# Performance work log

Measured on AMD Instinct MI355X. Metric: run time of the kernel, lower is better.

Reference implementation:

```python
import jax, jax.numpy as jnp
import numpy as np

B, D, H, E, TOP_K = 4096, 1024, 4096, 8, 2
EPS = 2.220446049250313e-16  # float64 machine eps, as in the torch source


def setup_inputs() -> dict:
    key = jax.random.key(0)
    k0, k1, k2, k3 = jax.random.split(key, 4)
    x = jax.random.normal(k0, (B, 1, D), dtype=jnp.float32)
    # torch inits w_gate to zeros (degenerate ties in topk); use small random for a meaningful test
    w_gate = jax.random.normal(k1, (D, E), dtype=jnp.float32) * 0.02
    W1 = jax.random.normal(k2, (E, D, H), dtype=jnp.float32) * (1.0 / np.sqrt(D))
    b1 = jnp.zeros((E, H), dtype=jnp.float32)
    W2 = jax.random.normal(k3, (E, H, D), dtype=jnp.float32) * (1.0 / np.sqrt(H))
    b2 = jnp.zeros((E, D), dtype=jnp.float32)
    loss_coef = jnp.float32(0.01)
    return {"x": x, "w_gate": w_gate, "W1": W1, "b1": b1, "W2": W2, "b2": b2,
            "loss_coef": loss_coef}


def _cv_squared(v, eps=1e-10):
    # torch .var() is unbiased (ddof=1)
    return jnp.var(v, ddof=1) / (jnp.mean(v) ** 2 + eps)


def reference(x, w_gate, W1, b1, W2, b2, loss_coef):
    n_tok = x.shape[0]
    flat = x.reshape(n_tok, -1)                      # [B, D]

    # --- top-k gating ---
    logits = flat @ w_gate                           # [B, E]
    top_logits, top_idx = jax.lax.top_k(logits, TOP_K)
    top_gates = jax.nn.softmax(top_logits, axis=1)   # softmax over the top-k logits only
    gates = jnp.zeros_like(logits).at[jnp.arange(n_tok)[:, None], top_idx].set(top_gates)

    # --- load-balancing loss ---
    importance = gates.sum(axis=0)                               # [E]
    load = (gates > 0).sum(axis=0).astype(jnp.float32)           # [E]
    balancing_loss = (_cv_squared(importance) + _cv_squared(load)) * loss_coef

    # --- per-expert FFN (dense equivalent of sort/dispatch: zero gates kill non-routed terms) ---
    h = jax.nn.relu(jnp.einsum('bd,edh->beh', flat, W1) + b1)    # [B, E, H]
    o = jnp.einsum('beh,ehd->bed', h, W2) + b2                   # [B, E, D]

    # --- combine: sum_e gate * exp(expert_out), then log (exp/log trick) ---
    combined = jnp.einsum('bed,be->bd', jnp.exp(o), gates)       # [B, D]
    combined = jnp.where(combined == 0, EPS, combined)
    y = jnp.log(combined)
    return y, balancing_loss
```

## Files before the change

### kernel.cpp

```cpp
#include <hip/hip_runtime.h>


typedef __attribute__((ext_vector_type(8))) short short8;
typedef __attribute__((ext_vector_type(4))) float f32x4;

#define B_TOK 4096
#define D_DIM 1024
#define H_DIM 4096
#define N_EXP 8
#define H_HALF 2048

__device__ __forceinline__ unsigned short f2bf(float f) {
  unsigned int u = __float_as_uint(f);
  u += 0x7fffu + ((u >> 16) & 1u);
  return (unsigned short)(u >> 16);
}
__device__ __forceinline__ float bf2f(unsigned short s) {
  return __uint_as_float(((unsigned int)s) << 16);
}

__device__ __forceinline__ void async_ld16(const void* g, void* l) {
  __builtin_amdgcn_global_load_lds(
      (const __attribute__((address_space(1))) void*)g,
      (__attribute__((address_space(3))) void*)l, 16, 0, 0);
}

__global__ __launch_bounds__(256) void convert_x_kernel(const float* __restrict__ x,
                                                        unsigned short* __restrict__ xb) {
  const size_t i = ((size_t)blockIdx.x * 256 + threadIdx.x) * 4;
  float4 v = *(const float4*)(x + i);
  ushort4 r;
  r.x = f2bf(v.x); r.y = f2bf(v.y); r.z = f2bf(v.z); r.w = f2bf(v.w);
  *(ushort4*)(xb + i) = r;
}

__global__ __launch_bounds__(256) void gating_kernel(
    const float* __restrict__ x, const float* __restrict__ wg,
    int* __restrict__ tok_e, float* __restrict__ tok_g) {
  const int lane = threadIdx.x & 63;
  const int t = blockIdx.x * 4 + (threadIdx.x >> 6);
  const float* xr = x + (size_t)t * D_DIM;
  double acc[8] = {0, 0, 0, 0, 0, 0, 0, 0};
  for (int d = lane; d < D_DIM; d += 64) {
    double xv = (double)xr[d];
    const float4 w0 = *(const float4*)(wg + d * 8);
    const float4 w1 = *(const float4*)(wg + d * 8 + 4);
    acc[0] += xv * (double)w0.x; acc[1] += xv * (double)w0.y;
    acc[2] += xv * (double)w0.z; acc[3] += xv * (double)w0.w;
    acc[4] += xv * (double)w1.x; acc[5] += xv * (double)w1.y;
    acc[6] += xv * (double)w1.z; acc[7] += xv * (double)w1.w;
  }
#pragma unroll
  for (int e = 0; e < 8; ++e) {
    double v = acc[e];
#pragma unroll
    for (int m = 32; m > 0; m >>= 1) v += __shfl_xor(v, m, 64);
    acc[e] = v;
  }
  if (lane == 0) {
    double b1v = -1e300, b2v = -1e300;
    int i1 = 0, i2 = 0;
#pragma unroll
    for (int e = 0; e < 8; ++e) {
      double v = acc[e];
      if (v > b1v) { b2v = b1v; i2 = i1; b1v = v; i1 = e; }
      else if (v > b2v) { b2v = v; i2 = e; }
    }
    float ex = expf((float)b2v - (float)b1v);
    float den = 1.f + ex;
    tok_e[2 * t] = i1; tok_e[2 * t + 1] = i2;
    tok_g[2 * t] = 1.f / den; tok_g[2 * t + 1] = ex / den;
  }
}

__global__ __launch_bounds__(1024) void route_kernel(
    const int* __restrict__ tok_e, const float* __restrict__ tok_g,
    int* __restrict__ tok_p, int* __restrict__ bucket,
    int* __restrict__ counts, int* __restrict__ offs,
    const float* __restrict__ coef, float* __restrict__ loss_out) {
  __shared__ int wavecnt[16][8];
  __shared__ int wavebase[16][8];
  __shared__ int run[8];
  __shared__ float impl[8];
  const int tid = threadIdx.x, lane = tid & 63, wv = tid >> 6;
  if (tid < 8) { run[tid] = 0; impl[tid] = 0.f; }
  __syncthreads();
  for (int c = 0; c < 8; ++c) {
    const int i = c * 1024 + tid;
    const int e = tok_e[i];
    const float g = tok_g[i];
    int rank = 0;
#pragma unroll
    for (int ee = 0; ee < 8; ++ee) {
      unsigned long long m = __ballot(e == ee);
      if (e == ee) rank = __popcll(m & ((1ull << lane) - 1ull));
      float s = (e == ee) ? g : 0.f;
#pragma unroll
      for (int o = 32; o > 0; o >>= 1) s += __shfl_xor(s, o, 64);
      if (lane == 0) {
        wavecnt[wv][ee] = __popcll(m);
        impl[ee] += 0.f;
        atomicAdd(&impl[ee], s);
      }
    }
    __syncthreads();
    if (tid < 8) {
      int base = run[tid];
      for (int w = 0; w < 16; ++w) { wavebase[w][tid] = base; base += wavecnt[w][tid]; }
      run[tid] = base;
    }
    __syncthreads();
    const int pos = wavebase[wv][e] + rank;
    tok_p[i] = pos;
    bucket[e * B_TOK + pos] = i >> 1;
  }
  __syncthreads();
  if (tid == 0) {
    int o = 0;
    double mi = 0, ml = 0;
    for (int e = 0; e < 8; ++e) {
      counts[e] = run[e]; offs[e] = o; o += run[e];
      mi += (double)impl[e]; ml += (double)run[e];
    }
    offs[8] = o;
    mi *= 0.125; ml *= 0.125;
    double vi = 0, vl = 0;
    for (int e = 0; e < 8; ++e) {
      double di = (double)impl[e] - mi; vi += di * di;
      double dl = (double)run[e]  - ml; vl += dl * dl;
    }
    vi /= 7.0; vl /= 7.0;
    *loss_out = (float)((vi / (mi * mi + 1e-10) + vl / (ml * ml + 1e-10)) * (double)coef[0]);
  }
}

__global__ __launch_bounds__(256) void transpose_w_kernel(
    const float* __restrict__ W, unsigned short* __restrict__ Wt,
    int ND_src, int k_base, int n_base, int KD_out,
    size_t w_stride_e, size_t wt_stride_e) {
  const int e = blockIdx.z;
  const int kt = blockIdx.x * 64;
  const int nt = blockIdx.y * 64;
  const float* We = W + (size_t)e * w_stride_e + (size_t)(k_base + kt) * ND_src + n_base + nt;
  unsigned short* Wte = Wt + (size_t)e * wt_stride_e + (size_t)nt * KD_out + kt;
  __shared__ unsigned int Ul[64][36];
  const int t = threadIdx.x;
  const int cb = (t & 15) * 4;
#pragma unroll
  for (int j = 0; j < 2; ++j) {
    const int p = (t >> 4) + j * 16;
    float4 f0 = *(const float4*)(We + (size_t)(2 * p) * ND_src + cb);
    float4 f1 = *(const float4*)(We + (size_t)(2 * p + 1) * ND_src + cb);
#pragma unroll
    for (int i2 = 0; i2 < 4; ++i2) {
      unsigned int u = (unsigned int)f2bf(((const float*)&f0)[i2]) |
                       ((unsigned int)f2bf(((const float*)&f1)[i2]) << 16);
      Ul[cb + i2][p] = u;
    }
  }
  __syncthreads();
  const int on = t >> 2;
  const int om = (t & 3) * 8;
  uint4 a = *(const uint4*)&Ul[on][om];
  uint4 b = *(const uint4*)&Ul[on][om + 4];
  uint4* dst = (uint4*)(Wte + (size_t)on * KD_out + om * 2);
  dst[0] = a; dst[1] = b;
}

template <int KDIM, int NDIM, bool GATHER, bool RELU, bool ACCUM>
__global__ __launch_bounds__(256) void grouped_gemm(
    const unsigned short* __restrict__ A, const unsigned short* __restrict__ Bt,
    const float* __restrict__ bias, int biasN,
    const int* __restrict__ counts, const int* __restrict__ offs,
    const int* __restrict__ bucket, unsigned short* __restrict__ Out, int outN) {
  const int e = blockIdx.z;
  const int n_e = counts[e];
  const int row0 = blockIdx.y * 128;
  if (row0 >= n_e) return;
  const int m_cnt = min(128, n_e - row0);
  const int n0 = blockIdx.x * 128;
  const int slot0 = offs[e] + row0;

  __shared__ unsigned short Alds[128][32];
  __shared__ unsigned short Blds[128][32];
  __shared__ int toklds[128];

  const int tid = threadIdx.x;
  const int lane = tid & 63;
  const int wid = tid >> 6;
  const int q = lane >> 4, l15 = lane & 15;
  const int wm = (wid >> 1) * 64, wn = (wid & 1) * 64;

  if (GATHER) {
    if (tid < 128) toklds[tid] = bucket[e * B_TOK + row0 + min(tid, m_cnt - 1)];
    __syncthreads();
  }
  const int r0 = tid >> 2;
  const int kc = (tid & 3) * 8;
  size_t ga0, ga1;
  if (GATHER) {
    ga0 = (size_t)toklds[r0] * KDIM + kc;
    ga1 = (size_t)toklds[r0 + 64] * KDIM + kc;
  } else {
    ga0 = (size_t)(slot0 + min(r0, m_cnt - 1)) * KDIM + kc;
    ga1 = (size_t)(slot0 + min(r0 + 64, m_cnt - 1)) * KDIM + kc;
  }
  const unsigned short* bbase =
      Bt + (size_t)e * NDIM * KDIM + (size_t)(n0 + r0) * KDIM + kc;
  char* aldsw = (char*)Alds + wid * 1024;
  char* bldsw = (char*)Blds + wid * 1024;

  f32x4 acc[4][4] = {};
  for (int k0 = 0; k0 < KDIM; k0 += 32) {
    async_ld16(A + ga0 + k0, aldsw);
    async_ld16(A + ga1 + k0, aldsw + 4096);
    async_ld16(bbase + k0, bldsw);
    async_ld16(bbase + (size_t)64 * KDIM + k0, bldsw + 4096);
    __syncthreads();
    short8 af[4], bfr[4];
#pragma unroll
    for (int mi = 0; mi < 4; ++mi) af[mi] = *(const short8*)&Alds[wm + mi * 16 + l15][q * 8];
#pragma unroll
    for (int ni = 0; ni < 4; ++ni) bfr[ni] = *(const short8*)&Blds[wn + ni * 16 + l15][q * 8];
#pragma unroll
    for (int mi = 0; mi < 4; ++mi)
#pragma unroll
      for (int ni = 0; ni < 4; ++ni)
        acc[mi][ni] = __builtin_amdgcn_mfma_f32_16x16x32_bf16(af[mi], bfr[ni], acc[mi][ni], 0, 0, 0);
    __syncthreads();
  }

  const float* be = bias + (size_t)e * biasN + n0;
#pragma unroll
  for (int ni = 0; ni < 4; ++ni) {
    const int c = wn + ni * 16 + l15;
    const float bv = ACCUM ? 0.f : be[c];
#pragma unroll
    for (int mi = 0; mi < 4; ++mi) {
      const int rb = wm + mi * 16 + q * 4;
#pragma unroll
      for (int rg = 0; rg < 4; ++rg) {
        const int r = rb + rg;
        if (r < m_cnt) {
          float v = acc[mi][ni][rg] + bv;
          if (RELU) v = fmaxf(v, 0.f);
          unsigned short* op = Out + (size_t)(slot0 + r) * outN + n0 + c;
          if (ACCUM) v += bf2f(*op);
          *op = f2bf(v);
        }
      }
    }
  }
}

__device__ __forceinline__ float comb1(float a, float b, float g1, float g2) {
  float c = g1 * expf(a) + g2 * expf(b);
  if (c == 0.f) c = 2.220446049250313e-16f;
  return logf(c);
}

__global__ __launch_bounds__(256) void combine_kernel(
    const unsigned short* __restrict__ o_buf, const int* __restrict__ offs,
    const int* __restrict__ tok_e, const int* __restrict__ tok_p,
    const float* __restrict__ tok_g, float* __restrict__ y) {
  const int t = blockIdx.x;
  const int e1 = tok_e[2 * t], e2 = tok_e[2 * t + 1];
  const int s1 = offs[e1] + tok_p[2 * t];
  const int s2 = offs[e2] + tok_p[2 * t + 1];
  const float g1 = tok_g[2 * t], g2 = tok_g[2 * t + 1];
  const int i = threadIdx.x * 4;
  ushort4 a4 = *(const ushort4*)(o_buf + (size_t)s1 * D_DIM + i);
  ushort4 b4 = *(const ushort4*)(o_buf + (size_t)s2 * D_DIM + i);
  float4 r;
  r.x = comb1(bf2f(a4.x), bf2f(b4.x), g1, g2);
  r.y = comb1(bf2f(a4.y), bf2f(b4.y), g1, g2);
  r.z = comb1(bf2f(a4.z), bf2f(b4.z), g1, g2);
  r.w = comb1(bf2f(a4.w), bf2f(b4.w), g1, g2);
  *(float4*)(y + (size_t)t * D_DIM + i) = r;
}

extern "C" void kernel_launch(void* const* d_in, const int* in_sizes, int n_in,
                              void* d_out, int out_size, void* d_ws, size_t ws_size,
                              hipStream_t stream) {
  const float* x  = (const float*)d_in[0];
  const float* wg = (const float*)d_in[1];
  const float* W1 = (const float*)d_in[2];
  const float* b1 = (const float*)d_in[3];
  const float* W2 = (const float*)d_in[4];
  const float* b2 = (const float*)d_in[5];
  const float* cf = (const float*)d_in[6];
  float* y = (float*)d_out;

  char* w = (char*)d_ws;
  unsigned short* x_bf = (unsigned short*)(w);
  int*   counts = (int*)(w + 8388608);
  int*   offs   = (int*)(w + 8388672);
  int*   tok_e  = (int*)(w + 8388736);
  int*   tok_p  = (int*)(w + 8421504);
  float* tok_g  = (float*)(w + 8454272);
  int*   bucket = (int*)(w + 8487040);
  unsigned short* wt     = (unsigned short*)(w + 8618112);
  unsigned short* h_half = (unsigned short*)(w + 42172544);
  unsigned short* o_buf  = (unsigned short*)(w + 75726976);
  if (ws_size < 92504192) return;

  convert_x_kernel<<<4096, 256, 0, stream>>>(x, x_bf);
  gating_kernel<<<1024, 256, 0, stream>>>(x, wg, tok_e, tok_g);
  route_kernel<<<1, 1024, 0, stream>>>(tok_e, tok_g, tok_p, bucket, counts, offs,
                                       cf, y + (size_t)B_TOK * D_DIM);

  for (int p = 0; p < 2; ++p) {
    transpose_w_kernel<<<dim3(16, 32, 8), 256, 0, stream>>>(
        W1, wt, H_DIM, 0, p * H_HALF, D_DIM,
        (size_t)D_DIM * H_DIM, (size_t)H_HALF * D_DIM);
    grouped_gemm<D_DIM, H_HALF, true, true, false>
        <<<dim3(H_HALF / 128, 32, N_EXP), 256, 0, stream>>>(
            x_bf, wt, b1 + p * H_HALF, H_DIM, counts, offs, bucket, h_half, H_HALF);
    transpose_w_kernel<<<dim3(32, 16, 8), 256, 0, stream>>>(
        W2, wt, D_DIM, p * H_HALF, 0, H_HALF,
        (size_t)H_DIM * D_DIM, (size_t)D_DIM * H_HALF);
    if (p == 0)
      grouped_gemm<H_HALF, D_DIM, false, false, false>
          <<<dim3(D_DIM / 128, 32, N_EXP), 256, 0, stream>>>(
              h_half, wt, b2, D_DIM, counts, offs, bucket, o_buf, D_DIM);
    else
      grouped_gemm<H_HALF, D_DIM, false, false, true>
          <<<dim3(D_DIM / 128, 32, N_EXP), 256, 0, stream>>>(
              h_half, wt, b2, D_DIM, counts, offs, bucket, o_buf, D_DIM);
  }

  combine_kernel<<<4096, 256, 0, stream>>>(o_buf, offs, tok_e, tok_p, tok_g, y);
}
```

Baseline: 661.0 us.

## Double-buffer grouped GEMM with larger 256x128 tiles and 8-wave blocks

Rewrites the grouped expert GEMM so the next K-slice is loaded asynchronously into a second LDS buffer while the current one is computed, and each iteration covers K=64 instead of 32. Blocks grow to 512 threads and 256x128 output tiles, so each tile of the weight operand is reused across more token rows and the number of barriers per unit of work drops. The cost is more LDS per block, which may limit how many blocks fit on a CU, and more wasted rows for experts whose token count is not a multiple of 256.

```diff
diff --git a/kernel.cpp b/kernel.cpp
--- a/kernel.cpp
+++ b/kernel.cpp
@@ -167,77 +167,102 @@
   dst[0] = a; dst[1] = b;
 }
 
-template <int KDIM, int NDIM, bool GATHER, bool RELU, bool ACCUM>
-__global__ __launch_bounds__(256) void grouped_gemm(
+template <int KDIM, int NDIM, int BM, int BN, int WGM, int WGN,
+          bool GATHER, bool RELU, bool ACCUM>
+__global__ __launch_bounds__(512) void grouped_gemm(
     const unsigned short* __restrict__ A, const unsigned short* __restrict__ Bt,
     const float* __restrict__ bias, int biasN,
     const int* __restrict__ counts, const int* __restrict__ offs,
     const int* __restrict__ bucket, unsigned short* __restrict__ Out, int outN) {
+  constexpr int WAVE_M = BM / WGM;
+  constexpr int WAVE_N = BN / WGN;
+  constexpr int M_REP = WAVE_M / 16;
+  constexpr int N_REP = WAVE_N / 16;
+  constexpr int AJ = BM / 64;
+  constexpr int BJ = BN / 64;
+  constexpr int NT = KDIM / 64;
+  static_assert(WGM * WGN == 8, "8 waves");
+  static_assert(BM % 64 == 0 && BN % 64 == 0 && KDIM % 64 == 0, "");
+
   const int e = blockIdx.z;
   const int n_e = counts[e];
-  const int row0 = blockIdx.y * 128;
+  const int row0 = blockIdx.y * BM;
   if (row0 >= n_e) return;
-  const int m_cnt = min(128, n_e - row0);
-  const int n0 = blockIdx.x * 128;
+  const int m_cnt = min(BM, n_e - row0);
+  const int n0 = blockIdx.x * BN;
   const int slot0 = offs[e] + row0;
 
-  __shared__ unsigned short Alds[128][32];
-  __shared__ unsigned short Blds[128][32];
-  __shared__ int toklds[128];
+  __shared__ unsigned short Alds[2][BM][64];
+  __shared__ unsigned short Blds[2][BN][64];
 
   const int tid = threadIdx.x;
   const int lane = tid & 63;
   const int wid = tid >> 6;
   const int q = lane >> 4, l15 = lane & 15;
-  const int wm = (wid >> 1) * 64, wn = (wid & 1) * 64;
-
-  if (GATHER) {
-    if (tid < 128) toklds[tid] = bucket[e * B_TOK + row0 + min(tid, m_cnt - 1)];
+  const int wr = wid / WGN, wc = wid % WGN;
+
+  const int arow = tid >> 3;
+  const int acol = (tid & 7) * 8;
+  size_t gaA[AJ], gaB[BJ];
+#pragma unroll
+  for (int j = 0; j < AJ; ++j) {
+    const int r = min(j * 64 + arow, m_cnt - 1);
+    const int src = GATHER ? bucket[e * B_TOK + row0 + r] : (slot0 + r);
+    gaA[j] = (size_t)src * KDIM + acol;
+  }
+#pragma unroll
+  for (int j = 0; j < BJ; ++j)
+    gaB[j] = (size_t)e * NDIM * KDIM + (size_t)(n0 + j * 64 + arow) * KDIM + acol;
+
+  f32x4 acc[M_REP][N_REP] = {};
+
+  auto stage = [&](int buf, int k0) {
+    char* ab = (char*)&Alds[buf][0][0] + wid * 1024;
+    char* bb = (char*)&Blds[buf][0][0] + wid * 1024;
+#pragma unroll
+    for (int j = 0; j < AJ; ++j) async_ld16(A + gaA[j] + k0, ab + j * 8192);
+#pragma unroll
+    for (int j = 0; j < BJ; ++j) async_ld16(Bt + gaB[j] + k0, bb + j * 8192);
+  };
+
+  auto compute = [&](int buf) {
+#pragma unroll
+    for (int kk = 0; kk < 2; ++kk) {
+      short8 af[M_REP], bfr[N_REP];
+#pragma unroll
+      for (int mi = 0; mi < M_REP; ++mi)
+        af[mi] = *(const short8*)&Alds[buf][wr * WAVE_M + mi * 16 + l15][kk * 32 + q * 8];
+#pragma unroll
+      for (int ni = 0; ni < N_REP; ++ni)
+        bfr[ni] = *(const short8*)&Blds[buf][wc * WAVE_N + ni * 16 + l15][kk * 32 + q * 8];
+#pragma unroll
+      for (int mi = 0; mi < M_REP; ++mi)
+#pragma unroll
+        for (int ni = 0; ni < N_REP; ++ni)
+          acc[mi][ni] =
+              __builtin_amdgcn_mfma_f32_16x16x32_bf16(af[mi], bfr[ni], acc[mi][ni], 0, 0, 0);
+    }
+  };
+
+  stage(0, 0);
+  __syncthreads();
+  int cur = 0;
+  for (int t = 0; t < NT - 1; ++t) {
+    stage(cur ^ 1, (t + 1) * 64);
+    compute(cur);
     __syncthreads();
-  }
-  const int r0 = tid >> 2;
-  const int kc = (tid & 3) * 8;
-  size_t ga0, ga1;
-  if (GATHER) {
-    ga0 = (size_t)toklds[r0] * KDIM + kc;
-    ga1 = (size_t)toklds[r0 + 64] * KDIM + kc;
-  } else {
-    ga0 = (size_t)(slot0 + min(r0, m_cnt - 1)) * KDIM + kc;
-    ga1 = (size_t)(slot0 + min(r0 + 64, m_cnt - 1)) * KDIM + kc;
-  }
-  const unsigned short* bbase =
-      Bt + (size_t)e * NDIM * KDIM + (size_t)(n0 + r0) * KDIM + kc;
-  char* aldsw = (char*)Alds + wid * 1024;
-  char* bldsw = (char*)Blds + wid * 1024;
-
-  f32x4 acc[4][4] = {};
-  for (int k0 = 0; k0 < KDIM; k0 += 32) {
-    async_ld16(A + ga0 + k0, aldsw);
-    async_ld16(A + ga1 + k0, aldsw + 4096);
-    async_ld16(bbase + k0, bldsw);
-    async_ld16(bbase + (size_t)64 * KDIM + k0, bldsw + 4096);
-    __syncthreads();
-    short8 af[4], bfr[4];
-#pragma unroll
-    for (int mi = 0; mi < 4; ++mi) af[mi] = *(const short8*)&Alds[wm + mi * 16 + l15][q * 8];
-#pragma unroll
-    for (int ni = 0; ni < 4; ++ni) bfr[ni] = *(const short8*)&Blds[wn + ni * 16 + l15][q * 8];
-#pragma unroll
-    for (int mi = 0; mi < 4; ++mi)
-#pragma unroll
-      for (int ni = 0; ni < 4; ++ni)
-        acc[mi][ni] = __builtin_amdgcn_mfma_f32_16x16x32_bf16(af[mi], bfr[ni], acc[mi][ni], 0, 0, 0);
-    __syncthreads();
-  }
+    cur ^= 1;
+  }
+  compute(cur);
 
   const float* be = bias + (size_t)e * biasN + n0;
 #pragma unroll
-  for (int ni = 0; ni < 4; ++ni) {
-    const int c = wn + ni * 16 + l15;
+  for (int ni = 0; ni < N_REP; ++ni) {
+    const int c = wc * WAVE_N + ni * 16 + l15;
     const float bv = ACCUM ? 0.f : be[c];
 #pragma unroll
-    for (int mi = 0; mi < 4; ++mi) {
-      const int rb = wm + mi * 16 + q * 4;
+    for (int mi = 0; mi < M_REP; ++mi) {
+      const int rb = wr * WAVE_M + mi * 16 + q * 4;
 #pragma unroll
       for (int rg = 0; rg < 4; ++rg) {
         const int r = rb + rg;
@@ -313,19 +338,19 @@
     transpose_w_kernel<<<dim3(16, 32, 8), 256, 0, stream>>>(
         W1, wt, H_DIM, 0, p * H_HALF, D_DIM,
         (size_t)D_DIM * H_DIM, (size_t)H_HALF * D_DIM);
-    grouped_gemm<D_DIM, H_HALF, true, true, false>
-        <<<dim3(H_HALF / 128, 32, N_EXP), 256, 0, stream>>>(
+    grouped_gemm<D_DIM, H_HALF, 256, 128, 4, 2, true, true, false>
+        <<<dim3(H_HALF / 128, 16, N_EXP), 512, 0, stream>>>(
             x_bf, wt, b1 + p * H_HALF, H_DIM, counts, offs, bucket, h_half, H_HALF);
     transpose_w_kernel<<<dim3(32, 16, 8), 256, 0, stream>>>(
         W2, wt, D_DIM, p * H_HALF, 0, H_HALF,
         (size_t)H_DIM * D_DIM, (size_t)D_DIM * H_HALF);
     if (p == 0)
-      grouped_gemm<H_HALF, D_DIM, false, false, false>
-          <<<dim3(D_DIM / 128, 32, N_EXP), 256, 0, stream>>>(
+      grouped_gemm<H_HALF, D_DIM, 256, 128, 4, 2, false, false, false>
+          <<<dim3(D_DIM / 128, 16, N_EXP), 512, 0, stream>>>(
               h_half, wt, b2, D_DIM, counts, offs, bucket, o_buf, D_DIM);
     else
-      grouped_gemm<H_HALF, D_DIM, false, false, true>
-          <<<dim3(D_DIM / 128, 32, N_EXP), 256, 0, stream>>>(
+      grouped_gemm<H_HALF, D_DIM, 256, 128, 4, 2, false, false, true>
+          <<<dim3(D_DIM / 128, 16, N_EXP), 512, 0, stream>>>(
               h_half, wt, b2, D_DIM, counts, offs, bucket, o_buf, D_DIM);
   }
 
```

New measurement: 874.4 us. 32.3% more time.

## Fuse weight fp32-to-bf16 transpose into grouped GEMM B-tile loading

Applied to the files above, without the earlier changes.

Removes the separate transpose_w_kernel passes that converted W1/W2 to transposed bf16 in workspace. Each GEMM block now reads fp32 weights directly, register-prefetches the next k-slice, converts and packs them to bf16, and writes the transposed tile into LDS itself. This drops four kernel launches and the round trip through the transposed-weight buffer. In exchange the GEMM reads twice the bytes for weights, and each weight tile is re-read and re-converted by every row-block of the expert (up to 32), rather than once.

```diff
diff --git a/kernel.cpp b/kernel.cpp
--- a/kernel.cpp
+++ b/kernel.cpp
@@ -17,6 +17,9 @@
 }
 __device__ __forceinline__ float bf2f(unsigned short s) {
   return __uint_as_float(((unsigned int)s) << 16);
+}
+__device__ __forceinline__ unsigned int pack2bf(float lo, float hi) {
+  return (unsigned int)f2bf(lo) | ((unsigned int)f2bf(hi) << 16);
 }
 
 __device__ __forceinline__ void async_ld16(const void* g, void* l) {
@@ -134,42 +137,10 @@
   }
 }
 
-__global__ __launch_bounds__(256) void transpose_w_kernel(
-    const float* __restrict__ W, unsigned short* __restrict__ Wt,
-    int ND_src, int k_base, int n_base, int KD_out,
-    size_t w_stride_e, size_t wt_stride_e) {
-  const int e = blockIdx.z;
-  const int kt = blockIdx.x * 64;
-  const int nt = blockIdx.y * 64;
-  const float* We = W + (size_t)e * w_stride_e + (size_t)(k_base + kt) * ND_src + n_base + nt;
-  unsigned short* Wte = Wt + (size_t)e * wt_stride_e + (size_t)nt * KD_out + kt;
-  __shared__ unsigned int Ul[64][36];
-  const int t = threadIdx.x;
-  const int cb = (t & 15) * 4;
-#pragma unroll
-  for (int j = 0; j < 2; ++j) {
-    const int p = (t >> 4) + j * 16;
-    float4 f0 = *(const float4*)(We + (size_t)(2 * p) * ND_src + cb);
-    float4 f1 = *(const float4*)(We + (size_t)(2 * p + 1) * ND_src + cb);
-#pragma unroll
-    for (int i2 = 0; i2 < 4; ++i2) {
-      unsigned int u = (unsigned int)f2bf(((const float*)&f0)[i2]) |
-                       ((unsigned int)f2bf(((const float*)&f1)[i2]) << 16);
-      Ul[cb + i2][p] = u;
-    }
-  }
-  __syncthreads();
-  const int on = t >> 2;
-  const int om = (t & 3) * 8;
-  uint4 a = *(const uint4*)&Ul[on][om];
-  uint4 b = *(const uint4*)&Ul[on][om + 4];
-  uint4* dst = (uint4*)(Wte + (size_t)on * KD_out + om * 2);
-  dst[0] = a; dst[1] = b;
-}
-
-template <int KDIM, int NDIM, bool GATHER, bool RELU, bool ACCUM>
+template <int KDIM, int WROW, bool GATHER, bool RELU, bool ACCUM>
 __global__ __launch_bounds__(256) void grouped_gemm(
-    const unsigned short* __restrict__ A, const unsigned short* __restrict__ Bt,
+    const unsigned short* __restrict__ A, const float* __restrict__ W,
+    size_t wse, int k_base, int n_base,
     const float* __restrict__ bias, int biasN,
     const int* __restrict__ counts, const int* __restrict__ offs,
     const int* __restrict__ bucket, unsigned short* __restrict__ Out, int outN) {
@@ -205,17 +176,43 @@
     ga0 = (size_t)(slot0 + min(r0, m_cnt - 1)) * KDIM + kc;
     ga1 = (size_t)(slot0 + min(r0 + 64, m_cnt - 1)) * KDIM + kc;
   }
-  const unsigned short* bbase =
-      Bt + (size_t)e * NDIM * KDIM + (size_t)(n0 + r0) * KDIM + kc;
   char* aldsw = (char*)Alds + wid * 1024;
-  char* bldsw = (char*)Blds + wid * 1024;
+
+  const int kp = tid & 15;
+  const int nb = tid >> 4;
+  const float* wb = W + (size_t)e * wse +
+                    ((size_t)(k_base + 2 * kp)) * WROW + n_base + n0 + nb * 8;
+
+  float4 c0, c1, c2, c3;
+  float4 p0, p1, p2, p3;
+  {
+    c0 = *(const float4*)(wb);
+    c1 = *(const float4*)(wb + 4);
+    c2 = *(const float4*)(wb + WROW);
+    c3 = *(const float4*)(wb + WROW + 4);
+  }
 
   f32x4 acc[4][4] = {};
+  unsigned int* bl = (unsigned int*)Blds;
+
+#pragma unroll 2
   for (int k0 = 0; k0 < KDIM; k0 += 32) {
     async_ld16(A + ga0 + k0, aldsw);
     async_ld16(A + ga1 + k0, aldsw + 4096);
-    async_ld16(bbase + k0, bldsw);
-    async_ld16(bbase + (size_t)64 * KDIM + k0, bldsw + 4096);
+    if (k0 + 32 < KDIM) {
+      const float* wn_ = wb + (size_t)(k0 + 32) * WROW;
+      p0 = *(const float4*)(wn_);
+      p1 = *(const float4*)(wn_ + 4);
+      p2 = *(const float4*)(wn_ + WROW);
+      p3 = *(const float4*)(wn_ + WROW + 4);
+    }
+#pragma unroll
+    for (int i = 0; i < 4; ++i) {
+      unsigned int lo = pack2bf(((const float*)&c0)[i], ((const float*)&c2)[i]);
+      unsigned int hi = pack2bf(((const float*)&c1)[i], ((const float*)&c3)[i]);
+      bl[(nb * 8 + i) * 16 + kp] = lo;
+      bl[(nb * 8 + 4 + i) * 16 + kp] = hi;
+    }
     __syncthreads();
     short8 af[4], bfr[4];
 #pragma unroll
@@ -228,9 +225,10 @@
       for (int ni = 0; ni < 4; ++ni)
         acc[mi][ni] = __builtin_amdgcn_mfma_f32_16x16x32_bf16(af[mi], bfr[ni], acc[mi][ni], 0, 0, 0);
     __syncthreads();
-  }
-
-  const float* be = bias + (size_t)e * biasN + n0;
+    c0 = p0; c1 = p1; c2 = p2; c3 = p3;
+  }
+
+  const float* be = bias + (size_t)e * biasN + n_base + n0;
 #pragma unroll
   for (int ni = 0; ni < 4; ++ni) {
     const int c = wn + ni * 16 + l15;
@@ -299,7 +297,6 @@
   int*   tok_p  = (int*)(w + 8421504);
   float* tok_g  = (float*)(w + 8454272);
   int*   bucket = (int*)(w + 8487040);
-  unsigned short* wt     = (unsigned short*)(w + 8618112);
   unsigned short* h_half = (unsigned short*)(w + 42172544);
   unsigned short* o_buf  = (unsigned short*)(w + 75726976);
   if (ws_size < 92504192) return;
@@ -310,23 +307,20 @@
                                        cf, y + (size_t)B_TOK * D_DIM);
 
   for (int p = 0; p < 2; ++p) {
-    transpose_w_kernel<<<dim3(16, 32, 8), 256, 0, stream>>>(
-        W1, wt, H_DIM, 0, p * H_HALF, D_DIM,
-        (size_t)D_DIM * H_DIM, (size_t)H_HALF * D_DIM);
-    grouped_gemm<D_DIM, H_HALF, true, true, false>
+    grouped_gemm<D_DIM, H_DIM, true, true, false>
         <<<dim3(H_HALF / 128, 32, N_EXP), 256, 0, stream>>>(
-            x_bf, wt, b1 + p * H_HALF, H_DIM, counts, offs, bucket, h_half, H_HALF);
-    transpose_w_kernel<<<dim3(32, 16, 8), 256, 0, stream>>>(
-        W2, wt, D_DIM, p * H_HALF, 0, H_HALF,
-        (size_t)H_DIM * D_DIM, (size_t)D_DIM * H_HALF);
+            x_bf, W1, (size_t)D_DIM * H_DIM, 0, p * H_HALF,
+            b1, H_DIM, counts, offs, bucket, h_half, H_HALF);
     if (p == 0)
       grouped_gemm<H_HALF, D_DIM, false, false, false>
           <<<dim3(D_DIM / 128, 32, N_EXP), 256, 0, stream>>>(
-              h_half, wt, b2, D_DIM, counts, offs, bucket, o_buf, D_DIM);
+              h_half, W2, (size_t)H_DIM * D_DIM, p * H_HALF, 0,
+              b2, D_DIM, counts, offs, bucket, o_buf, D_DIM);
     else
       grouped_gemm<H_HALF, D_DIM, false, false, true>
           <<<dim3(D_DIM / 128, 32, N_EXP), 256, 0, stream>>>(
-              h_half, wt, b2, D_DIM, counts, offs, bucket, o_buf, D_DIM);
+              h_half, W2, (size_t)H_DIM * D_DIM, p * H_HALF, 0,
+              b2, D_DIM, counts, offs, bucket, o_buf, D_DIM);
   }
 
   combine_kernel<<<4096, 256, 0, stream>>>(o_buf, offs, tok_e, tok_p, tok_g, y);
```

Result: slower. 974.6 us (+47.4%).
